# Performance work log

Hardware: AMD Instinct MI355X
Metric: run time of the kernel (lower is better)

Reference implementation:

```python
import jax, jax.numpy as jnp
import numpy as np

B, D_IN, HD, HN = 16384, 1024, 128, 8
D = HD * HN  # 1024
PROJ = int((4.0 / 3.0) * D)  # 1365
EPS = 1e-5


def setup_inputs() -> dict:
    key = jax.random.key(0)
    ks = jax.random.split(key, 16)
    s = 0.02
    inp = {
        'seq': jax.random.normal(ks[0], (B, D_IN), jnp.float32),
        'c0': jnp.zeros((B, D), jnp.float32),
        'n0': jnp.ones((B, D), jnp.float32),
        'h0': jax.random.normal(ks[1], (B, D), jnp.float32) * 0.1,
        'm0': jnp.zeros((B, D), jnp.float32),
        'ln_w': jnp.ones((D_IN,), jnp.float32),
        'ln_b': jnp.zeros((D_IN,), jnp.float32),
        'Wz': jax.random.normal(ks[2], (D, D_IN), jnp.float32) * s,
        'bz': jnp.zeros((D,), jnp.float32),
        'Wi': jax.random.normal(ks[3], (D, D_IN), jnp.float32) * s,
        'bi': jnp.zeros((D,), jnp.float32),
        'Wo': jax.random.normal(ks[4], (D, D_IN), jnp.float32) * s,
        'bo': jnp.zeros((D,), jnp.float32),
        'Wf': jax.random.normal(ks[5], (D, D_IN), jnp.float32) * s,
        'bf': jnp.zeros((D,), jnp.float32),
        'Rz': jax.random.normal(ks[6], (HN, HD, HD), jnp.float32) * s,
        'Ri': jax.random.normal(ks[7], (HN, HD, HD), jnp.float32) * s,
        'Ro': jax.random.normal(ks[8], (HN, HD, HD), jnp.float32) * s,
        'Rf': jax.random.normal(ks[9], (HN, HD, HD), jnp.float32) * s,
        'gn_w': jnp.ones((D,), jnp.float32),
        'gn_b': jnp.zeros((D,), jnp.float32),
        'up_w': jax.random.normal(ks[10], (2 * PROJ, D), jnp.float32) * s,
        'up_b': jnp.zeros((2 * PROJ,), jnp.float32),
        'down_w': jax.random.normal(ks[11], (D_IN, PROJ), jnp.float32) * s,
        'down_b': jnp.zeros((D_IN,), jnp.float32),
    }
    return inp


def _layernorm(x, w, b):
    mu = jnp.mean(x, axis=-1, keepdims=True)
    var = jnp.mean(jnp.square(x - mu), axis=-1, keepdims=True)
    return (x - mu) * jax.lax.rsqrt(var + EPS) * w + b


def _groupnorm(x, w, b):
    # x: (B, D) -> groups of HD channels per head
    xr = x.reshape(x.shape[0], HN, HD)
    mu = jnp.mean(xr, axis=-1, keepdims=True)
    var = jnp.mean(jnp.square(xr - mu), axis=-1, keepdims=True)
    xn = ((xr - mu) * jax.lax.rsqrt(var + EPS)).reshape(x.shape)
    return xn * w + b


def _block_linear(h, R):
    # block-diagonal recurrence: per-head (HD,HD) matmul
    hr = h.reshape(h.shape[0], HN, HD)
    return jnp.einsum('hed,bhd->bhe', R, hr).reshape(h.shape)


def reference(seq, c0, n0, h0, m0, ln_w, ln_b, Wz, bz, Wi, bi, Wo, bo, Wf, bf,
              Rz, Ri, Ro, Rf, gn_w, gn_b, up_w, up_b, down_w, down_b):
    x_t = _layernorm(seq, ln_w, ln_b)
    x_c = x_t  # use_conv=False default path
    i_t = x_c @ Wi.T + bi + _block_linear(h0, Ri)
    f_t = x_c @ Wf.T + bf + _block_linear(h0, Rf)
    z_t = x_t @ Wz.T + bz + _block_linear(h0, Rz)
    o_t = x_t @ Wo.T + bo + _block_linear(h0, Ro)
    m_t = jnp.maximum(f_t + m0, i_t)
    i_e = jnp.exp(i_t - m_t)
    f_e = jnp.exp(f_t - m_t + m0)
    z_a = jnp.tanh(z_t)
    o_a = jax.nn.sigmoid(o_t)
    c_t = f_e * c0 + i_e * z_a
    n_t = f_e * n0 + i_e
    h_t = o_a * (c_t / n_t)
    out = _groupnorm(h_t, gn_w, gn_b)
    up = out @ up_w.T + up_b
    out1, out2 = jnp.split(up, 2, axis=-1)
    out = out1 + jax.nn.gelu(out2, approximate=False)
    out = out @ down_w.T + down_b
    return (out + seq, c_t, n_t, h_t, m_t)
```

## Files before the change

### kernel.cpp

```cpp
#include <hip/hip_runtime.h>
#include <hip/hip_bf16.h>
#include <cstdint>
#include <type_traits>

typedef __attribute__((ext_vector_type(8))) __bf16 bf16x8;
typedef __attribute__((ext_vector_type(8))) short short8;
typedef __attribute__((ext_vector_type(4))) float f32x4;
using u16 = unsigned short;

template <typename T, typename = void> struct mfma_ok : std::false_type {};
template <typename T>
struct mfma_ok<T, std::void_t<decltype(__builtin_amdgcn_mfma_f32_16x16x32_bf16(
    std::declval<T>(), std::declval<T>(), std::declval<f32x4>(), 0, 0, 0))>>
    : std::true_type {};
using frag_t = std::conditional_t<mfma_ok<bf16x8>::value, bf16x8, short8>;
static_assert(sizeof(frag_t) == 16, "frag must be 4 VGPRs");

template <typename T>
__device__ __forceinline__ f32x4 MFMA(T a, T b, f32x4 c) {
  return __builtin_amdgcn_mfma_f32_16x16x32_bf16(a, b, c, 0, 0, 0);
}

__device__ __forceinline__ void gl_lds16(const u16* g, u16* l) {
  __builtin_amdgcn_global_load_lds(
      (const __attribute__((address_space(1))) unsigned int*)g,
      (__attribute__((address_space(3))) unsigned int*)l, 16, 0, 0);
}

__device__ __forceinline__ u16 f2bf(float v) {
  __hip_bfloat16 h = __float2bfloat16(v);
  return __builtin_bit_cast(u16, h);
}

__device__ __forceinline__ int xcd_swz(int wid, int nwg) {
  return (wid & 7) * (nwg >> 3) + (wid >> 3);
}

__device__ __forceinline__ void gemm256(
    const u16* __restrict__ A, int lda,
    const u16* __restrict__ B, int ldb, int K,
    u16* lds, f32x4 (&acc)[8][4])
{
  const int t = threadIdx.x;
  const int l = t & 63;
  const int w = t >> 6;
  const int wm = w >> 2, wc = w & 3;

  const int sc = (t & 7) ^ ((t >> 3) & 7);
  const u16* gA = A + (t >> 3) * lda + sc * 8;
  const u16* gB = B + (t >> 3) * ldb + sc * 8;

  const int lr = l & 15;
  const int lk = l >> 4;
  const int lx = l & 7;
  const int pk0 = ((0 + lk) ^ lx) * 8;
  const int pk1 = ((4 + lk) ^ lx) * 8;
  const int arow0 = (wm * 128 + lr) * 64;
  const int brow0 = 16384 + (wc * 64 + lr) * 64;

  const int nt = K >> 6;

#define STAGE(buf, kt) do {                                   \
    const u16* a_ = gA + (kt) * 64;                           \
    const u16* b_ = gB + (kt) * 64;                           \
    u16* s_ = (buf);                                          \
    gl_lds16(a_,             s_ + w * 512);                   \
    gl_lds16(a_ +  64 * lda, s_ +  4096 + w * 512);           \
    gl_lds16(a_ + 128 * lda, s_ +  8192 + w * 512);           \
    gl_lds16(a_ + 192 * lda, s_ + 12288 + w * 512);           \
    gl_lds16(b_,             s_ + 16384 + w * 512);           \
    gl_lds16(b_ +  64 * ldb, s_ + 20480 + w * 512);           \
    gl_lds16(b_ + 128 * ldb, s_ + 24576 + w * 512);           \
    gl_lds16(b_ + 192 * ldb, s_ + 28672 + w * 512);           \
  } while (0)

  STAGE(lds, 0);
  asm volatile("s_waitcnt vmcnt(0)" ::: "memory");
  __builtin_amdgcn_s_barrier();

  for (int kt = 0; kt < nt; ++kt) {
    u16* cur = lds + (kt & 1) * 32768;
    u16* nxt = lds + ((kt + 1) & 1) * 32768;
    if (kt + 1 < nt) STAGE(nxt, kt + 1);
    __builtin_amdgcn_sched_barrier(0);
#pragma unroll
    for (int kf = 0; kf < 2; ++kf) {
      const int pk = kf ? pk1 : pk0;
      frag_t a[8], b[4];
#pragma unroll
      for (int fm = 0; fm < 8; ++fm)
        a[fm] = *(const frag_t*)(cur + arow0 + fm * 1024 + pk);
#pragma unroll
      for (int fn = 0; fn < 4; ++fn)
        b[fn] = *(const frag_t*)(cur + brow0 + fn * 1024 + pk);
      __builtin_amdgcn_s_setprio(1);
#pragma unroll
      for (int fn = 0; fn < 4; ++fn)
#pragma unroll
        for (int fm = 0; fm < 8; ++fm)
          acc[fm][fn] = MFMA(a[fm], b[fn], acc[fm][fn]);
      __builtin_amdgcn_s_setprio(0);
    }
    asm volatile("s_waitcnt vmcnt(0)" ::: "memory");
    __builtin_amdgcn_s_barrier();
  }
#undef STAGE
}

__global__ __launch_bounds__(256) void prep_ln_kernel(
    const float* __restrict__ seq, const float* __restrict__ h0,
    const float* __restrict__ lnw, const float* __restrict__ lnb,
    const float* __restrict__ Wi, const float* __restrict__ Wf,
    const float* __restrict__ Wz, const float* __restrict__ Wo,
    const float* __restrict__ Ri, const float* __restrict__ Rf,
    const float* __restrict__ Rz, const float* __restrict__ Ro,
    const float* __restrict__ upw, const float* __restrict__ dnw,
    u16* __restrict__ xb, u16* __restrict__ h0b,
    u16* __restrict__ Wcat2, u16* __restrict__ upint, u16* __restrict__ dnp)
{
  const int t = threadIdx.x;
  if (blockIdx.x < 16384) {
    const int row = blockIdx.x;
    const float4 v = ((const float4*)(seq + (size_t)row * 1024))[t];
    float s = v.x + v.y + v.z + v.w;
    float q = v.x * v.x + v.y * v.y + v.z * v.z + v.w * v.w;
#pragma unroll
    for (int o = 32; o >= 1; o >>= 1) { s += __shfl_xor(s, o); q += __shfl_xor(q, o); }
    __shared__ float sm[8];
    const int l = t & 63, w = t >> 6;
    if (l == 0) { sm[w] = s; sm[4 + w] = q; }
    __syncthreads();
    s = sm[0] + sm[1] + sm[2] + sm[3];
    q = sm[4] + sm[5] + sm[6] + sm[7];
    const float mu = s * (1.f / 1024.f);
    const float var = q * (1.f / 1024.f) - mu * mu;
    const float rstd = rsqrtf(var + 1e-5f);
    const float4 wv = ((const float4*)lnw)[t];
    const float4 bv = ((const float4*)lnb)[t];
    ushort4 o4;
    o4.x = f2bf((v.x - mu) * rstd * wv.x + bv.x);
    o4.y = f2bf((v.y - mu) * rstd * wv.y + bv.y);
    o4.z = f2bf((v.z - mu) * rstd * wv.z + bv.z);
    o4.w = f2bf((v.w - mu) * rstd * wv.w + bv.w);
    ((ushort4*)(xb + (size_t)row * 1024))[t] = o4;
    const float4 h = ((const float4*)(h0 + (size_t)row * 1024))[t];
    ushort4 h4;
    h4.x = f2bf(h.x); h4.y = f2bf(h.y); h4.z = f2bf(h.z); h4.w = f2bf(h.w);
    ((ushort4*)(h0b + (size_t)row * 1024))[t] = h4;
    return;
  }
  const int stride = 2048 * 256;
  for (int i = (blockIdx.x - 16384) * 256 + t; i < 9043968; i += stride) {
    if (i < 4718592) {
      const int s = i / 294912;
      const int rem = i - s * 294912;
      const int vcol = rem / 1152;
      const int k = rem - vcol * 1152;
      const int wc = vcol >> 6, gsel = (vcol >> 4) & 3, c16 = vcol & 15;
      float v;
      if (k < 1024) {
        const int col = s * 64 + wc * 16 + c16;
        const float* W = (gsel == 0) ? Wi : (gsel == 1) ? Wf : (gsel == 2) ? Wz : Wo;
        v = W[col * 1024 + k];
      } else {
        const int head = s >> 1;
        const int colInHead = (s & 1) * 64 + wc * 16 + c16;
        const float* R = (gsel == 0) ? Ri : (gsel == 1) ? Rf : (gsel == 2) ? Rz : Ro;
        v = R[head * 16384 + colInHead * 128 + (k - 1024)];
      }
      Wcat2[i] = f2bf(v);
    } else if (i < 7602176) {
      const int j = i - 4718592;
      const int vcol = j >> 10, k = j & 1023;
      const int tile = vcol >> 8, wc = (vcol >> 6) & 3;
      const int half = (vcol >> 5) & 1, c32 = vcol & 31;
      const int a = tile * 128 + wc * 32 + c32;
      upint[j] = (a < 1365) ? f2bf(upw[(half * 1365 + a) * 1024 + k]) : (u16)0;
    } else {
      const int j = i - 7602176;
      const int row = j / 1408, k = j - row * 1408;
      dnp[j] = (k < 1365) ? f2bf(dnw[row * 1365 + k]) : (u16)0;
    }
  }
}

__global__ __launch_bounds__(256, 2) void gate_kernel(
    const u16* __restrict__ xb, const u16* __restrict__ h0b,
    const u16* __restrict__ Wcat2,
    const float* __restrict__ bi, const float* __restrict__ bfv,
    const float* __restrict__ bz, const float* __restrict__ bo,
    const float* __restrict__ c0, const float* __restrict__ n0i,
    const float* __restrict__ m0,
    float* __restrict__ oc, float* __restrict__ on,
    float* __restrict__ oh, float* __restrict__ om)
{
  __shared__ __align__(16) u16 lds[24576];
  const int t = threadIdx.x;
  const int l = t & 63;
  const int w = t >> 6;

  const int wid = xcd_swz(blockIdx.x, 2048);
  const int s = wid & 15;
  const int mt = wid >> 4;
  const int head = s >> 1;

  const u16* Agl = xb + (size_t)mt * 131072;
  const u16* Hgl = h0b + (size_t)mt * 131072 + head * 128;
  const u16* Bgl = Wcat2 + s * 294912;

  const int gsw = ((t & 3) ^ ((t >> 3) & 3)) * 8;
  const int sr = t >> 2;

  const int lr = l & 15, lk = l >> 4;
  const int ck = (lk ^ ((lr >> 1) & 3)) * 8;

  f32x4 acc[8][4] = {};

#define GSTG(buf, kt) do {                                                 \
    const u16* Ab = ((kt) < 32) ? (Agl + (kt) * 32) : (Hgl + ((kt) - 32) * 32); \
    const u16* Bb = Bgl + (kt) * 32;                                       \
    u16* s_ = (buf);                                                       \
    gl_lds16(Ab + sr * 1024 + gsw,          s_ + w * 512);                 \
    gl_lds16(Ab + (64 + sr) * 1024 + gsw,   s_ + 2048 + w * 512);          \
    gl_lds16(Bb + sr * 1152 + gsw,          s_ + 4096 + w * 512);          \
    gl_lds16(Bb + (64 + sr) * 1152 + gsw,   s_ + 6144 + w * 512);          \
    gl_lds16(Bb + (128 + sr) * 1152 + gsw,  s_ + 8192 + w * 512);          \
    gl_lds16(Bb + (192 + sr) * 1152 + gsw,  s_ + 10240 + w * 512);         \
  } while (0)

  GSTG(lds, 0);
  asm volatile("s_waitcnt vmcnt(0)" ::: "memory");
  __builtin_amdgcn_s_barrier();

  for (int kt = 0; kt < 36; ++kt) {
    u16* cur = lds + (kt & 1) * 12288;
    u16* nxt = lds + ((kt + 1) & 1) * 12288;
    const bool more = (kt + 1 < 36);
    if (more) GSTG(nxt, kt + 1);

    frag_t a[8], b[4];
#pragma unroll
    for (int fm = 0; fm < 8; ++fm)
      a[fm] = *(const frag_t*)(cur + (fm * 16 + lr) * 32 + ck);
#pragma unroll
    for (int fn = 0; fn < 4; ++fn)
      b[fn] = *(const frag_t*)(cur + 4096 + (w * 64 + fn * 16 + lr) * 32 + ck);
#pragma unroll
    for (int fn = 0; fn < 4; ++fn)
#pragma unroll
      for (int fm = 0; fm < 8; ++fm)
        acc[fm][fn] = MFMA(a[fm], b[fn], acc[fm][fn]);

    if (more) asm volatile("s_waitcnt vmcnt(0)" ::: "memory");
    __builtin_amdgcn_s_barrier();
  }
#undef GSTG

  const int cc = s * 64 + w * 16 + lr;
  const float biv = bi[cc], bfvv = bfv[cc], bzv = bz[cc], bov = bo[cc];
#pragma unroll
  for (int fm = 0; fm < 8; ++fm) {
    const int rbase = mt * 128 + fm * 16 + lk * 4;
#pragma unroll
    for (int r = 0; r < 4; ++r) {
      const size_t idx = (size_t)(rbase + r) * 1024 + cc;
      const float it = acc[fm][0][r] + biv;
      const float ft = acc[fm][1][r] + bfvv;
      const float zt = acc[fm][2][r] + bzv;
      const float ot = acc[fm][3][r] + bov;
      const float mp = m0[idx];
      const float mt_ = fmaxf(ft + mp, it);
      const float ie = __expf(it - mt_);
      const float fe = __expf(ft - mt_ + mp);
      const float ct = fe * c0[idx] + ie * tanhf(zt);
      const float nt = fe * n0i[idx] + ie;
      const float ht = (ct / nt) / (1.f + __expf(-ot));
      oc[idx] = ct; on[idx] = nt; oh[idx] = ht; om[idx] = mt_;
    }
  }
}

__global__ __launch_bounds__(256) void gn_kernel(
    const float* __restrict__ h, const float* __restrict__ gw,
    const float* __restrict__ gb, u16* __restrict__ gnb)
{
  const int t = threadIdx.x, l = t & 63, w = t >> 6;
  for (int grp = blockIdx.x * 4 + w; grp < 16384 * 8; grp += gridDim.x * 4) {
    const int b = grp >> 3, hd = grp & 7;
    const float2 v = ((const float2*)(h + b * 1024 + hd * 128))[l];
    float s = v.x + v.y, q = v.x * v.x + v.y * v.y;
#pragma unroll
    for (int o = 32; o >= 1; o >>= 1) { s += __shfl_xor(s, o); q += __shfl_xor(q, o); }
    const float mu = s * (1.f / 128.f);
    const float var = q * (1.f / 128.f) - mu * mu;
    const float rstd = rsqrtf(var + 1e-5f);
    const float2 wv = ((const float2*)(gw + hd * 128))[l];
    const float2 bv = ((const float2*)(gb + hd * 128))[l];
    ushort2 o2;
    o2.x = f2bf((v.x - mu) * rstd * wv.x + bv.x);
    o2.y = f2bf((v.y - mu) * rstd * wv.y + bv.y);
    ((ushort2*)(gnb + b * 1024 + hd * 128))[l] = o2;
  }
}

__global__ __launch_bounds__(512, 2) void up_kernel(
    const u16* __restrict__ gnb, const u16* __restrict__ upint,
    const float* __restrict__ upb, u16* __restrict__ g)
{
  __shared__ __align__(16) u16 lds[65536];
  const int wid = xcd_swz(blockIdx.x, 704);
  const int vt = wid % 11, mt = wid / 11;
  const int m0r = mt * 256;
  f32x4 acc[8][4] = {};
  gemm256(gnb + (size_t)m0r * 1024, 1024, upint + vt * 262144, 1024, 1024,
          lds, acc);
  const int t = threadIdx.x, l = t & 63, w = t >> 6, wm = w >> 2, wc = w & 3;
#pragma unroll
  for (int fm = 0; fm < 8; ++fm) {
    const int rbase = m0r + wm * 128 + fm * 16 + (l >> 4) * 4;
#pragma unroll
    for (int fn = 0; fn < 2; ++fn) {
      const int a = vt * 128 + wc * 32 + fn * 16 + (l & 15);
      const float b1 = (a < 1365) ? upb[a] : 0.f;
      const float b2 = (a < 1365) ? upb[1365 + a] : 0.f;
#pragma unroll
      for (int r = 0; r < 4; ++r) {
        const float u1 = acc[fm][fn][r] + b1;
        const float u2 = acc[fm][fn + 2][r] + b2;
        const float ge = 0.5f * u2 * (1.f + erff(u2 * 0.70710678118654752f));
        g[(size_t)(rbase + r) * 1408 + a] = f2bf(u1 + ge);
      }
    }
  }
}

__global__ __launch_bounds__(512, 2) void down_kernel(
    const u16* __restrict__ g, const u16* __restrict__ dnp,
    const float* __restrict__ dnb, const float* __restrict__ seq,
    float* __restrict__ out)
{
  __shared__ __align__(16) u16 lds[65536];
  const int wid = xcd_swz(blockIdx.x, 256);
  const int nc = (wid & 3) * 256;
  const int m0r = (wid >> 2) * 256;
  f32x4 acc[8][4] = {};
  gemm256(g + (size_t)m0r * 1408, 1408, dnp + nc * 1408, 1408, 1408, lds, acc);
  const int t = threadIdx.x, l = t & 63, w = t >> 6, wm = w >> 2, wc = w & 3;
#pragma unroll
  for (int fm = 0; fm < 8; ++fm) {
    const int rbase = m0r + wm * 128 + fm * 16 + (l >> 4) * 4;
#pragma unroll
    for (int fn = 0; fn < 4; ++fn) {
      const int cc = nc + wc * 64 + fn * 16 + (l & 15);
      const float bb = dnb[cc];
#pragma unroll
      for (int r = 0; r < 4; ++r) {
        const size_t idx = (size_t)(rbase + r) * 1024 + cc;
        out[idx] = acc[fm][fn][r] + bb + seq[idx];
      }
    }
  }
}

extern "C" void kernel_launch(void* const* d_in, const int* in_sizes, int n_in,
                              void* d_out, int out_size, void* d_ws, size_t ws_size,
                              hipStream_t stream) {
  const float* seq = (const float*)d_in[0];
  const float* c0  = (const float*)d_in[1];
  const float* n0i = (const float*)d_in[2];
  const float* h0  = (const float*)d_in[3];
  const float* m0  = (const float*)d_in[4];
  const float* lnw = (const float*)d_in[5];
  const float* lnb = (const float*)d_in[6];
  const float* Wz  = (const float*)d_in[7];
  const float* bz  = (const float*)d_in[8];
  const float* Wi  = (const float*)d_in[9];
  const float* bi  = (const float*)d_in[10];
  const float* Wo  = (const float*)d_in[11];
  const float* bo  = (const float*)d_in[12];
  const float* Wf  = (const float*)d_in[13];
  const float* bf_ = (const float*)d_in[14];
  const float* Rz  = (const float*)d_in[15];
  const float* Ri  = (const float*)d_in[16];
  const float* Ro  = (const float*)d_in[17];
  const float* Rf  = (const float*)d_in[18];
  const float* gw  = (const float*)d_in[19];
  const float* gb  = (const float*)d_in[20];
  const float* upw = (const float*)d_in[21];
  const float* upb = (const float*)d_in[22];
  const float* dnw = (const float*)d_in[23];
  const float* dnb = (const float*)d_in[24];

  char* ws = (char*)d_ws;
  u16* xb    = (u16*)(ws);
  u16* h0b   = (u16*)(ws + 33554432);
  u16* Wcat2 = (u16*)(ws + 67108864);
  u16* upc   = (u16*)(ws + 76546048);
  u16* dnp   = (u16*)(ws + 82313216);
  u16* g     = (u16*)(ws + 85196800);

  float* out = (float*)d_out;
  float* oc = out + 16777216;
  float* on = out + 2 * 16777216;
  float* oh = out + 3 * 16777216;
  float* om = out + 4 * 16777216;

  prep_ln_kernel<<<dim3(18432), dim3(256), 0, stream>>>(
      seq, h0, lnw, lnb, Wi, Wf, Wz, Wo, Ri, Rf, Rz, Ro, upw, dnw,
      xb, h0b, Wcat2, upc, dnp);
  gate_kernel<<<dim3(2048), dim3(256), 0, stream>>>(
      xb, h0b, Wcat2, bi, bf_, bz, bo, c0, n0i, m0, oc, on, oh, om);
  gn_kernel<<<dim3(2048), dim3(256), 0, stream>>>(oh, gw, gb, xb);
  up_kernel<<<dim3(704), dim3(512), 0, stream>>>(xb, upc, upb, g);
  down_kernel<<<dim3(256), dim3(512), 0, stream>>>(g, dnp, dnb, seq, out);
}
```

Before: 525.6 us.

## Pack gate GEMM operands in MFMA fragment order and load directly to registers

The prep kernel now writes the layer-normed input, h0 and the concatenated gate weights in an MFMA-fragment-packed order, so each lane's 16-byte fragment sits contiguously. The gate kernel drops its LDS staging and barriers and loads fragments straight from global memory into double-buffered registers. Each block now computes a 128x64 tile with a 2x2 wave grid, which doubles the grid size and raises the occupancy hint to 3. This removes LDS traffic and synchronisation, but operands shared between waves are now fetched twice from global memory and rely on the caches for reuse.

```diff
diff --git a/kernel.cpp b/kernel.cpp
--- a/kernel.cpp
+++ b/kernel.cpp
@@ -115,8 +115,8 @@
     const float* __restrict__ Ri, const float* __restrict__ Rf,
     const float* __restrict__ Rz, const float* __restrict__ Ro,
     const float* __restrict__ upw, const float* __restrict__ dnw,
-    u16* __restrict__ xb, u16* __restrict__ h0b,
-    u16* __restrict__ Wcat2, u16* __restrict__ upint, u16* __restrict__ dnp)
+    u16* __restrict__ xh, u16* __restrict__ hpk,
+    u16* __restrict__ wpk, u16* __restrict__ upint, u16* __restrict__ dnp)
 {
   const int t = threadIdx.x;
   if (blockIdx.x < 16384) {
@@ -142,33 +142,39 @@
     o4.y = f2bf((v.y - mu) * rstd * wv.y + bv.y);
     o4.z = f2bf((v.z - mu) * rstd * wv.z + bv.z);
     o4.w = f2bf((v.w - mu) * rstd * wv.w + bv.w);
-    ((ushort4*)(xb + (size_t)row * 1024))[t] = o4;
+    const int k0 = t * 4;
+    const int mt = row >> 7, g = (row & 127) >> 4, r15 = row & 15;
+    size_t dst = ((size_t)(mt * 32 + (k0 >> 5)) * 8 + g) * 512 +
+                 (((k0 & 31) >> 3) * 16 + r15) * 8 + (k0 & 7);
+    *(ushort4*)(xh + dst) = o4;
     const float4 h = ((const float4*)(h0 + (size_t)row * 1024))[t];
     ushort4 h4;
     h4.x = f2bf(h.x); h4.y = f2bf(h.y); h4.z = f2bf(h.z); h4.w = f2bf(h.w);
-    ((ushort4*)(h0b + (size_t)row * 1024))[t] = h4;
+    const int hd = k0 >> 7, kh = k0 & 127;
+    dst = ((size_t)((hd * 128 + mt) * 4 + (kh >> 5)) * 8 + g) * 512 +
+          (((kh & 31) >> 3) * 16 + r15) * 8 + (kh & 7);
+    *(ushort4*)(hpk + dst) = h4;
     return;
   }
   const int stride = 2048 * 256;
   for (int i = (blockIdx.x - 16384) * 256 + t; i < 9043968; i += stride) {
     if (i < 4718592) {
-      const int s = i / 294912;
-      const int rem = i - s * 294912;
-      const int vcol = rem / 1152;
-      const int k = rem - vcol * 1152;
-      const int wc = vcol >> 6, gsel = (vcol >> 4) & 3, c16 = vcol & 15;
+      const int u = i >> 9, off = i & 511;
+      const int l = off >> 3, j = off & 7;
+      const int g = u & 7, q = u >> 3;
+      const int kt = q % 36, nv = q / 36;
+      const int wc = g >> 2, fn = g & 3;
+      const int cc = (nv >> 1) * 64 + ((nv & 1) * 2 + wc) * 16 + (l & 15);
+      const int k = kt * 32 + (l >> 4) * 8 + j;
       float v;
       if (k < 1024) {
-        const int col = s * 64 + wc * 16 + c16;
-        const float* W = (gsel == 0) ? Wi : (gsel == 1) ? Wf : (gsel == 2) ? Wz : Wo;
-        v = W[col * 1024 + k];
+        const float* W = (fn == 0) ? Wi : (fn == 1) ? Wf : (fn == 2) ? Wz : Wo;
+        v = W[cc * 1024 + k];
       } else {
-        const int head = s >> 1;
-        const int colInHead = (s & 1) * 64 + wc * 16 + c16;
-        const float* R = (gsel == 0) ? Ri : (gsel == 1) ? Rf : (gsel == 2) ? Rz : Ro;
-        v = R[head * 16384 + colInHead * 128 + (k - 1024)];
+        const float* R = (fn == 0) ? Ri : (fn == 1) ? Rf : (fn == 2) ? Rz : Ro;
+        v = R[(nv >> 2) * 16384 + (cc & 127) * 128 + (k - 1024)];
       }
-      Wcat2[i] = f2bf(v);
+      wpk[i] = f2bf(v);
     } else if (i < 7602176) {
       const int j = i - 4718592;
       const int vcol = j >> 10, k = j & 1023;
@@ -184,9 +190,9 @@
   }
 }
 
-__global__ __launch_bounds__(256, 2) void gate_kernel(
-    const u16* __restrict__ xb, const u16* __restrict__ h0b,
-    const u16* __restrict__ Wcat2,
+__global__ __launch_bounds__(256, 3) void gate_kernel(
+    const u16* __restrict__ xh, const u16* __restrict__ hpk,
+    const u16* __restrict__ wpk,
     const float* __restrict__ bi, const float* __restrict__ bfv,
     const float* __restrict__ bz, const float* __restrict__ bo,
     const float* __restrict__ c0, const float* __restrict__ n0i,
@@ -194,73 +200,49 @@
     float* __restrict__ oc, float* __restrict__ on,
     float* __restrict__ oh, float* __restrict__ om)
 {
-  __shared__ __align__(16) u16 lds[24576];
-  const int t = threadIdx.x;
-  const int l = t & 63;
-  const int w = t >> 6;
-
-  const int wid = xcd_swz(blockIdx.x, 2048);
-  const int s = wid & 15;
-  const int mt = wid >> 4;
-  const int head = s >> 1;
-
-  const u16* Agl = xb + (size_t)mt * 131072;
-  const u16* Hgl = h0b + (size_t)mt * 131072 + head * 128;
-  const u16* Bgl = Wcat2 + s * 294912;
-
-  const int gsw = ((t & 3) ^ ((t >> 3) & 3)) * 8;
-  const int sr = t >> 2;
+  const int t = threadIdx.x, l = t & 63, w = t >> 6;
+  const int wm = w >> 1, wc = w & 1;
+  const int wid = xcd_swz(blockIdx.x, 4096);
+  const int nv = wid & 31, mt = wid >> 5;
+  const int head = nv >> 2;
+
+  const u16* Abase = xh  + ((size_t)(mt * 32) * 8 + wm * 4) * 512 + l * 8;
+  const u16* Hbase = hpk + ((size_t)((head * 128 + mt) * 4) * 8 + wm * 4) * 512 + l * 8;
+  const u16* Bbase = wpk + ((size_t)(nv * 36) * 8 + wc * 4) * 512 + l * 8;
+
+  f32x4 acc[4][4] = {};
+  frag_t a[2][4], b[2][4];
+
+#define LOADSET(s, kt) do {                                                \
+    const u16* ap_ = ((kt) < 32) ? (Abase + (size_t)(kt) * 4096)           \
+                                 : (Hbase + (size_t)((kt) - 32) * 4096);   \
+    const u16* bp_ = Bbase + (size_t)(kt) * 4096;                          \
+    _Pragma("unroll")                                                      \
+    for (int f = 0; f < 4; ++f) {                                          \
+      a[s][f] = *(const frag_t*)(ap_ + f * 512);                           \
+      b[s][f] = *(const frag_t*)(bp_ + f * 512);                           \
+    }                                                                      \
+  } while (0)
+
+  LOADSET(0, 0);
+#pragma unroll 2
+  for (int kt = 0; kt < 36; ++kt) {
+    if (kt + 1 < 36) LOADSET((kt + 1) & 1, kt + 1);
+    const int s = kt & 1;
+#pragma unroll
+    for (int fn = 0; fn < 4; ++fn)
+#pragma unroll
+      for (int fm = 0; fm < 4; ++fm)
+        acc[fm][fn] = MFMA(a[s][fm], b[s][fn], acc[fm][fn]);
+  }
+#undef LOADSET
 
   const int lr = l & 15, lk = l >> 4;
-  const int ck = (lk ^ ((lr >> 1) & 3)) * 8;
-
-  f32x4 acc[8][4] = {};
-
-#define GSTG(buf, kt) do {                                                 \
-    const u16* Ab = ((kt) < 32) ? (Agl + (kt) * 32) : (Hgl + ((kt) - 32) * 32); \
-    const u16* Bb = Bgl + (kt) * 32;                                       \
-    u16* s_ = (buf);                                                       \
-    gl_lds16(Ab + sr * 1024 + gsw,          s_ + w * 512);                 \
-    gl_lds16(Ab + (64 + sr) * 1024 + gsw,   s_ + 2048 + w * 512);          \
-    gl_lds16(Bb + sr * 1152 + gsw,          s_ + 4096 + w * 512);          \
-    gl_lds16(Bb + (64 + sr) * 1152 + gsw,   s_ + 6144 + w * 512);          \
-    gl_lds16(Bb + (128 + sr) * 1152 + gsw,  s_ + 8192 + w * 512);          \
-    gl_lds16(Bb + (192 + sr) * 1152 + gsw,  s_ + 10240 + w * 512);         \
-  } while (0)
-
-  GSTG(lds, 0);
-  asm volatile("s_waitcnt vmcnt(0)" ::: "memory");
-  __builtin_amdgcn_s_barrier();
-
-  for (int kt = 0; kt < 36; ++kt) {
-    u16* cur = lds + (kt & 1) * 12288;
-    u16* nxt = lds + ((kt + 1) & 1) * 12288;
-    const bool more = (kt + 1 < 36);
-    if (more) GSTG(nxt, kt + 1);
-
-    frag_t a[8], b[4];
-#pragma unroll
-    for (int fm = 0; fm < 8; ++fm)
-      a[fm] = *(const frag_t*)(cur + (fm * 16 + lr) * 32 + ck);
-#pragma unroll
-    for (int fn = 0; fn < 4; ++fn)
-      b[fn] = *(const frag_t*)(cur + 4096 + (w * 64 + fn * 16 + lr) * 32 + ck);
-#pragma unroll
-    for (int fn = 0; fn < 4; ++fn)
-#pragma unroll
-      for (int fm = 0; fm < 8; ++fm)
-        acc[fm][fn] = MFMA(a[fm], b[fn], acc[fm][fn]);
-
-    if (more) asm volatile("s_waitcnt vmcnt(0)" ::: "memory");
-    __builtin_amdgcn_s_barrier();
-  }
-#undef GSTG
-
-  const int cc = s * 64 + w * 16 + lr;
+  const int cc = (nv >> 1) * 64 + ((nv & 1) * 2 + wc) * 16 + lr;
   const float biv = bi[cc], bfvv = bfv[cc], bzv = bz[cc], bov = bo[cc];
 #pragma unroll
-  for (int fm = 0; fm < 8; ++fm) {
-    const int rbase = mt * 128 + fm * 16 + lk * 4;
+  for (int fm = 0; fm < 4; ++fm) {
+    const int rbase = mt * 128 + wm * 64 + fm * 16 + lk * 4;
 #pragma unroll
     for (int r = 0; r < 4; ++r) {
       const size_t idx = (size_t)(rbase + r) * 1024 + cc;
@@ -392,12 +374,12 @@
   const float* dnb = (const float*)d_in[24];
 
   char* ws = (char*)d_ws;
-  u16* xb    = (u16*)(ws);
-  u16* h0b   = (u16*)(ws + 33554432);
-  u16* Wcat2 = (u16*)(ws + 67108864);
-  u16* upc   = (u16*)(ws + 76546048);
-  u16* dnp   = (u16*)(ws + 82313216);
-  u16* g     = (u16*)(ws + 85196800);
+  u16* xh  = (u16*)(ws);
+  u16* hpk = (u16*)(ws + 33554432);
+  u16* wpk = (u16*)(ws + 67108864);
+  u16* upc = (u16*)(ws + 76546048);
+  u16* dnp = (u16*)(ws + 82313216);
+  u16* g   = (u16*)(ws + 85196800);
 
   float* out = (float*)d_out;
   float* oc = out + 16777216;
@@ -407,10 +389,10 @@
 
   prep_ln_kernel<<<dim3(18432), dim3(256), 0, stream>>>(
       seq, h0, lnw, lnb, Wi, Wf, Wz, Wo, Ri, Rf, Rz, Ro, upw, dnw,
-      xb, h0b, Wcat2, upc, dnp);
-  gate_kernel<<<dim3(2048), dim3(256), 0, stream>>>(
-      xb, h0b, Wcat2, bi, bf_, bz, bo, c0, n0i, m0, oc, on, oh, om);
-  gn_kernel<<<dim3(2048), dim3(256), 0, stream>>>(oh, gw, gb, xb);
-  up_kernel<<<dim3(704), dim3(512), 0, stream>>>(xb, upc, upb, g);
+      xh, hpk, wpk, upc, dnp);
+  gate_kernel<<<dim3(4096), dim3(256), 0, stream>>>(
+      xh, hpk, wpk, bi, bf_, bz, bo, c0, n0i, m0, oc, on, oh, om);
+  gn_kernel<<<dim3(2048), dim3(256), 0, stream>>>(oh, gw, gb, xh);
+  up_kernel<<<dim3(704), dim3(512), 0, stream>>>(xh, upc, upb, g);
   down_kernel<<<dim3(256), dim3(512), 0, stream>>>(g, dnp, dnb, seq, out);
 }
```

New measurement: 631.5 us. 20.1% more time.
